# Optimization experiments

Hardware: AMD Instinct MI355X
Metric: run time of the kernel (lower is better)

The kernel has to match this reference:

```python
import jax, jax.numpy as jnp
import numpy as np

N_ATOMS = 50000
N_PAIRS = 1000000
F = 64


def setup_inputs() -> dict:
    key = jax.random.key(0)
    ks = jax.random.split(key, 9)
    return {
        "per_atom_scalar_representation": jax.random.normal(ks[0], (N_ATOMS, 1, F), dtype=jnp.float32),
        "per_atom_vector_representation": jax.random.normal(ks[1], (N_ATOMS, 3, F), dtype=jnp.float32),
        "W_ij": jax.random.normal(ks[2], (N_PAIRS, 3 * F), dtype=jnp.float32),
        "dir_ij": jax.random.normal(ks[3], (N_PAIRS, 3), dtype=jnp.float32),
        "pairlist": jax.random.randint(ks[4], (2, N_PAIRS), 0, N_ATOMS, dtype=jnp.int64),
        # interatomic_net params: Dense(F->F, silu) then Dense(F->3F)
        "W1": jax.random.normal(ks[5], (F, F), dtype=jnp.float32) / np.sqrt(F),
        "b1": jnp.zeros((F,), dtype=jnp.float32),
        "W2": jax.random.normal(ks[6], (F, 3 * F), dtype=jnp.float32) / np.sqrt(F),
        "b2": jnp.zeros((3 * F,), dtype=jnp.float32),
    }


def reference(per_atom_scalar_representation, per_atom_vector_representation,
              W_ij, dir_ij, pairlist, W1, b1, W2, b2):
    n_atoms = per_atom_scalar_representation.shape[0]
    f = W1.shape[0]
    idx_i, idx_j = pairlist[0], pairlist[1]

    # interatomic_net: Dense(F->F, silu) -> Dense(F->3F)
    h = jax.nn.silu(per_atom_scalar_representation @ W1 + b1)   # [N,1,F]
    t = h @ W2 + b2                                              # [N,1,3F]

    s_j = t[idx_j]                                               # [P,1,3F] gather
    weighted_s_j = W_ij[:, None, :] * s_j                        # [P,1,3F]
    ds1, ds2, ds3 = jnp.split(weighted_s_j, 3, axis=-1)          # each [P,1,F]

    ds_i = jax.ops.segment_sum(ds1, idx_i, num_segments=n_atoms)  # [N,1,F]
    q = per_atom_scalar_representation + ds_i

    v_j = per_atom_vector_representation[idx_j]                  # [P,3,F]
    dmu = ds2 * dir_ij[:, :, None] + ds3 * v_j                   # [P,3,F]
    dv_i = jax.ops.segment_sum(dmu, idx_i, num_segments=n_atoms)  # [N,3,F]
    mu = per_atom_vector_representation + dv_i
    return (q, mu)
```

## Files before the change

kernel.cpp:

```cpp
#include <hip/hip_runtime.h>

#define FDIM 64
#define TFDIM 192
#define MLP_A 8

static __device__ __forceinline__ float bf2f(unsigned short u) {
    union { unsigned int i; float f; } x;
    x.i = ((unsigned int)u) << 16;
    return x.f;
}
static __device__ __forceinline__ unsigned short f2bf(float f) {
    unsigned int u = __float_as_uint(f);
    unsigned int rounding = 0x7fffu + ((u >> 16) & 1u);
    return (unsigned short)((u + rounding) >> 16);
}

__global__ void zero_kernel(int* __restrict__ count, int n) {
    int i = blockIdx.x * blockDim.x + threadIdx.x;
    if (i < n) count[i] = 0;
}

__global__ void cvt_kernel(const float* __restrict__ v, unsigned short* __restrict__ v16,
                           int n_elems) {
    int g = blockIdx.x * blockDim.x + threadIdx.x;
    int n4 = n_elems >> 2;
    if (g < n4) {
        float4 x = ((const float4*)v)[g];
        ushort4 y;
        y.x = f2bf(x.x); y.y = f2bf(x.y); y.z = f2bf(x.z); y.w = f2bf(x.w);
        ((ushort4*)v16)[g] = y;
    }
}

__global__ __launch_bounds__(64) void mlp_kernel(
    const float* __restrict__ s, const float* __restrict__ W1,
    const float* __restrict__ b1, const float* __restrict__ W2,
    const float* __restrict__ b2, unsigned short* __restrict__ t16, int n_atoms) {
    __shared__ float s_lds[MLP_A][FDIM];
    __shared__ float h_lds[MLP_A][FDIM];
    const int f = threadIdx.x;
    const int atom0 = blockIdx.x * MLP_A;

#pragma unroll
    for (int a = 0; a < MLP_A; ++a) {
        int atom = atom0 + a;
        int ac = atom < n_atoms ? atom : (n_atoms - 1);
        s_lds[a][f] = s[(size_t)ac * FDIM + f];
    }
    __syncthreads();

    float acc[MLP_A];
#pragma unroll
    for (int a = 0; a < MLP_A; ++a) acc[a] = b1[f];
    for (int k = 0; k < FDIM; ++k) {
        float w = W1[k * FDIM + f];
#pragma unroll
        for (int a = 0; a < MLP_A; ++a) acc[a] = fmaf(s_lds[a][k], w, acc[a]);
    }
#pragma unroll
    for (int a = 0; a < MLP_A; ++a)
        h_lds[a][f] = acc[a] / (1.0f + __expf(-acc[a]));
    __syncthreads();

    float o0[MLP_A], o1[MLP_A], o2[MLP_A];
#pragma unroll
    for (int a = 0; a < MLP_A; ++a) {
        o0[a] = b2[f]; o1[a] = b2[FDIM + f]; o2[a] = b2[2 * FDIM + f];
    }
    for (int k = 0; k < FDIM; ++k) {
        float w0 = W2[k * TFDIM + f];
        float w1 = W2[k * TFDIM + FDIM + f];
        float w2 = W2[k * TFDIM + 2 * FDIM + f];
#pragma unroll
        for (int a = 0; a < MLP_A; ++a) {
            float h = h_lds[a][k];
            o0[a] = fmaf(h, w0, o0[a]);
            o1[a] = fmaf(h, w1, o1[a]);
            o2[a] = fmaf(h, w2, o2[a]);
        }
    }
#pragma unroll
    for (int a = 0; a < MLP_A; ++a) {
        int atom = atom0 + a;
        if (atom < n_atoms) {
            size_t base = (size_t)atom * TFDIM;
            t16[base + f] = f2bf(o0[a]);
            t16[base + FDIM + f] = f2bf(o1[a]);
            t16[base + 2 * FDIM + f] = f2bf(o2[a]);
        }
    }
}

__global__ void hist_kernel(const int* __restrict__ idx_i, int* __restrict__ count, int n_pairs) {
    int n4 = n_pairs >> 2;
    for (int g = blockIdx.x * blockDim.x + threadIdx.x; g < n4; g += gridDim.x * blockDim.x) {
        int4 ii = ((const int4*)idx_i)[g];
        atomicAdd(&count[ii.x], 1);
        atomicAdd(&count[ii.y], 1);
        atomicAdd(&count[ii.z], 1);
        atomicAdd(&count[ii.w], 1);
    }
    if (blockIdx.x == 0 && threadIdx.x == 0) {
        for (int p = n4 << 2; p < n_pairs; ++p) atomicAdd(&count[idx_i[p]], 1);
    }
}

__global__ __launch_bounds__(1024) void scan_local(const int* __restrict__ count,
                                                   int* __restrict__ offsets,
                                                   int* __restrict__ bsum, int n) {
    __shared__ int wsum[16];
    const int tid = threadIdx.x;
    const int lane = tid & 63, wid = tid >> 6;
    int i = blockIdx.x * 1024 + tid;
    int val = (i < n) ? count[i] : 0;
    int x = val;
#pragma unroll
    for (int off = 1; off < 64; off <<= 1) {
        int y = __shfl_up(x, off);
        if (lane >= off) x += y;
    }
    if (lane == 63) wsum[wid] = x;
    __syncthreads();
    if (wid == 0) {
        int w = (lane < 16) ? wsum[lane] : 0;
#pragma unroll
        for (int off = 1; off < 16; off <<= 1) {
            int y = __shfl_up(w, off);
            if (lane >= off) w += y;
        }
        if (lane < 16) wsum[lane] = w;
    }
    __syncthreads();
    int excl = x - val + (wid ? wsum[wid - 1] : 0);
    if (i < n) offsets[i] = excl;
    if (tid == 0) bsum[blockIdx.x] = wsum[15];
}

__global__ __launch_bounds__(64) void scan_tops(int* __restrict__ bsum,
                                                int* __restrict__ offsets, int nb, int n) {
    const int lane = threadIdx.x;
    int val = (lane < nb) ? bsum[lane] : 0;
    int x = val;
#pragma unroll
    for (int off = 1; off < 64; off <<= 1) {
        int y = __shfl_up(x, off);
        if (lane >= off) x += y;
    }
    if (lane < nb) bsum[lane] = x - val;
    if (lane == 63) offsets[n] = x;
}

__global__ void scan_add(int* __restrict__ offsets, const int* __restrict__ bsum, int n) {
    int i = blockIdx.x * blockDim.x + threadIdx.x;
    if (i < n) offsets[i] += bsum[i >> 10];
}

__global__ void scatter_kernel(const int* __restrict__ idx_i, const int* __restrict__ idx_j,
                               const float* __restrict__ dir, int* __restrict__ offsets,
                               int2* __restrict__ pjbuf, float4* __restrict__ dbuf,
                               int n_pairs) {
    int n4 = n_pairs >> 2;
    const float4* dir4 = (const float4*)dir;
    for (int g = blockIdx.x * blockDim.x + threadIdx.x; g < n4; g += gridDim.x * blockDim.x) {
        int4 ii = ((const int4*)idx_i)[g];
        int4 jj = ((const int4*)idx_j)[g];
        float4 da = dir4[3 * g];
        float4 db = dir4[3 * g + 1];
        float4 dc = dir4[3 * g + 2];
        int p0 = 4 * g;
        int pos;
        pos = atomicAdd(&offsets[ii.x], 1);
        pjbuf[pos] = make_int2(p0 + 0, jj.x);
        dbuf[pos] = make_float4(da.x, da.y, da.z, 0.f);
        pos = atomicAdd(&offsets[ii.y], 1);
        pjbuf[pos] = make_int2(p0 + 1, jj.y);
        dbuf[pos] = make_float4(da.w, db.x, db.y, 0.f);
        pos = atomicAdd(&offsets[ii.z], 1);
        pjbuf[pos] = make_int2(p0 + 2, jj.z);
        dbuf[pos] = make_float4(db.z, db.w, dc.x, 0.f);
        pos = atomicAdd(&offsets[ii.w], 1);
        pjbuf[pos] = make_int2(p0 + 3, jj.w);
        dbuf[pos] = make_float4(dc.y, dc.z, dc.w, 0.f);
    }
    if (blockIdx.x == 0 && threadIdx.x == 0) {
        for (int p = n4 << 2; p < n_pairs; ++p) {
            int pos = atomicAdd(&offsets[idx_i[p]], 1);
            pjbuf[pos] = make_int2(p, idx_j[p]);
            dbuf[pos] = make_float4(dir[3 * (size_t)p], dir[3 * (size_t)p + 1],
                                    dir[3 * (size_t)p + 2], 0.f);
        }
    }
}

__global__ __launch_bounds__(256) void main_kernel(
    const float* __restrict__ s, const float* __restrict__ v,
    const float* __restrict__ Wij, const unsigned short* __restrict__ v16,
    const unsigned short* __restrict__ t16, const int* __restrict__ offsets_post,
    const int* __restrict__ count, const int2* __restrict__ pjbuf,
    const float4* __restrict__ dbuf,
    float* __restrict__ q_out, float* __restrict__ mu_out, int n_atoms) {
    const int w = threadIdx.x >> 6;
    const int f = threadIdx.x & 63;
    const int i = blockIdx.x * 4 + w;
    if (i >= n_atoms) return;
    const int end = offsets_post[i];
    const int cnt = count[i];
    const int start = end - cnt;

    float accq = 0.f, acc0 = 0.f, acc1 = 0.f, acc2 = 0.f;
    for (int cbase = start; cbase < end; cbase += 64) {
        int m = end - cbase;
        if (m > 64) m = 64;
        int idx = cbase + f;
        int sidx = idx < end ? idx : start;
        int2 pj = pjbuf[sidx];
        float4 dd = dbuf[sidx];
#pragma unroll 2
        for (int k = 0; k < m; ++k) {
            int p = __builtin_amdgcn_readlane(pj.x, k);
            int j = __builtin_amdgcn_readlane(pj.y, k);
            float d0 = __uint_as_float(__builtin_amdgcn_readlane(__float_as_uint(dd.x), k));
            float d1 = __uint_as_float(__builtin_amdgcn_readlane(__float_as_uint(dd.y), k));
            float d2 = __uint_as_float(__builtin_amdgcn_readlane(__float_as_uint(dd.z), k));
            const float* wp = Wij + (size_t)p * TFDIM;
            const unsigned short* tp = t16 + (size_t)j * TFDIM;
            const unsigned short* vp = v16 + (size_t)j * TFDIM;
            float w1 = __builtin_nontemporal_load(wp + f);
            float w2 = __builtin_nontemporal_load(wp + FDIM + f);
            float w3 = __builtin_nontemporal_load(wp + 2 * FDIM + f);
            float t1 = bf2f(tp[f]);
            float t2 = bf2f(tp[FDIM + f]);
            float t3 = bf2f(tp[2 * FDIM + f]);
            float v0 = bf2f(vp[f]);
            float v1 = bf2f(vp[FDIM + f]);
            float v2 = bf2f(vp[2 * FDIM + f]);
            float ds2 = w2 * t2;
            float ds3 = w3 * t3;
            accq = fmaf(w1, t1, accq);
            acc0 = fmaf(ds2, d0, fmaf(ds3, v0, acc0));
            acc1 = fmaf(ds2, d1, fmaf(ds3, v1, acc1));
            acc2 = fmaf(ds2, d2, fmaf(ds3, v2, acc2));
        }
    }

    size_t qb = (size_t)i * FDIM;
    size_t vb = (size_t)i * TFDIM;
    __builtin_nontemporal_store(s[qb + f] + accq, &q_out[qb + f]);
    __builtin_nontemporal_store(v[vb + f] + acc0, &mu_out[vb + f]);
    __builtin_nontemporal_store(v[vb + FDIM + f] + acc1, &mu_out[vb + FDIM + f]);
    __builtin_nontemporal_store(v[vb + 2 * FDIM + f] + acc2, &mu_out[vb + 2 * FDIM + f]);
}

extern "C" void kernel_launch(void* const* d_in, const int* in_sizes, int n_in,
                              void* d_out, int out_size, void* d_ws, size_t ws_size,
                              hipStream_t stream) {
    const float* s   = (const float*)d_in[0];
    const float* v   = (const float*)d_in[1];
    const float* Wij = (const float*)d_in[2];
    const float* dir = (const float*)d_in[3];
    const int*   pl  = (const int*)d_in[4];
    const float* W1  = (const float*)d_in[5];
    const float* b1  = (const float*)d_in[6];
    const float* W2  = (const float*)d_in[7];
    const float* b2  = (const float*)d_in[8];

    const int n_atoms = in_sizes[0] / FDIM;
    const int n_pairs = in_sizes[3] / 3;
    const int* idx_i = pl;
    const int* idx_j = pl + n_pairs;

    char* ws = (char*)d_ws;
    size_t off = 0;
    auto alloc = [&](size_t bytes) {
        void* ptr = ws + off;
        off = (off + bytes + 15) & ~(size_t)15;
        return ptr;
    };
    unsigned short* t16 = (unsigned short*)alloc((size_t)n_atoms * TFDIM * 2);
    unsigned short* v16 = (unsigned short*)alloc((size_t)n_atoms * TFDIM * 2);
    int* count   = (int*)alloc((size_t)n_atoms * 4);
    int* offsets = (int*)alloc(((size_t)n_atoms + 1) * 4);
    int* bsum    = (int*)alloc(64 * 4);
    int2* pjbuf  = (int2*)alloc((size_t)n_pairs * 8);
    float4* dbuf = (float4*)alloc((size_t)n_pairs * 16);

    float* q_out  = (float*)d_out;
    float* mu_out = q_out + (size_t)n_atoms * FDIM;

    const int nb = (n_atoms + 1023) / 1024;
    const int nv = n_atoms * TFDIM;

    zero_kernel<<<(n_atoms + 255) / 256, 256, 0, stream>>>(count, n_atoms);
    cvt_kernel<<<((nv >> 2) + 255) / 256, 256, 0, stream>>>(v, v16, nv);
    mlp_kernel<<<(n_atoms + MLP_A - 1) / MLP_A, 64, 0, stream>>>(s, W1, b1, W2, b2, t16, n_atoms);
    hist_kernel<<<1024, 256, 0, stream>>>(idx_i, count, n_pairs);
    scan_local<<<nb, 1024, 0, stream>>>(count, offsets, bsum, n_atoms);
    scan_tops<<<1, 64, 0, stream>>>(bsum, offsets, nb, n_atoms);
    scan_add<<<(n_atoms + 1023) / 1024, 1024, 0, stream>>>(offsets, bsum, n_atoms);
    scatter_kernel<<<1024, 256, 0, stream>>>(idx_i, idx_j, dir, offsets, pjbuf, dbuf, n_pairs);
    main_kernel<<<(n_atoms + 3) / 4, 256, 0, stream>>>(s, v, Wij, v16, t16, offsets, count,
                                                       pjbuf, dbuf, q_out, mu_out, n_atoms);
}
```

Measured before the change: 384.3 us.

## Interleave per-atom t and v bf16 data and pack pair records into one buffer

New measurement: 432.4 us. 12.5% more time.

```diff
diff --git a/kernel.cpp b/kernel.cpp
--- a/kernel.cpp
+++ b/kernel.cpp
@@ -4,15 +4,15 @@
 #define TFDIM 192
 #define MLP_A 8
 
-static __device__ __forceinline__ float bf2f(unsigned short u) {
+static __device__ __forceinline__ float bf2f(unsigned int u16) {
     union { unsigned int i; float f; } x;
-    x.i = ((unsigned int)u) << 16;
+    x.i = u16 << 16;
     return x.f;
 }
-static __device__ __forceinline__ unsigned short f2bf(float f) {
+static __device__ __forceinline__ unsigned int f2bf(float f) {
     unsigned int u = __float_as_uint(f);
     unsigned int rounding = 0x7fffu + ((u >> 16) & 1u);
-    return (unsigned short)((u + rounding) >> 16);
+    return (u + rounding) >> 16;
 }
 
 __global__ void zero_kernel(int* __restrict__ count, int n) {
@@ -20,22 +20,11 @@
     if (i < n) count[i] = 0;
 }
 
-__global__ void cvt_kernel(const float* __restrict__ v, unsigned short* __restrict__ v16,
-                           int n_elems) {
-    int g = blockIdx.x * blockDim.x + threadIdx.x;
-    int n4 = n_elems >> 2;
-    if (g < n4) {
-        float4 x = ((const float4*)v)[g];
-        ushort4 y;
-        y.x = f2bf(x.x); y.y = f2bf(x.y); y.z = f2bf(x.z); y.w = f2bf(x.w);
-        ((ushort4*)v16)[g] = y;
-    }
-}
-
 __global__ __launch_bounds__(64) void mlp_kernel(
-    const float* __restrict__ s, const float* __restrict__ W1,
-    const float* __restrict__ b1, const float* __restrict__ W2,
-    const float* __restrict__ b2, unsigned short* __restrict__ t16, int n_atoms) {
+    const float* __restrict__ s, const float* __restrict__ v,
+    const float* __restrict__ W1, const float* __restrict__ b1,
+    const float* __restrict__ W2, const float* __restrict__ b2,
+    uint4* __restrict__ tv, int n_atoms) {
     __shared__ float s_lds[MLP_A][FDIM];
     __shared__ float h_lds[MLP_A][FDIM];
     const int f = threadIdx.x;
@@ -83,10 +72,16 @@
     for (int a = 0; a < MLP_A; ++a) {
         int atom = atom0 + a;
         if (atom < n_atoms) {
-            size_t base = (size_t)atom * TFDIM;
-            t16[base + f] = f2bf(o0[a]);
-            t16[base + FDIM + f] = f2bf(o1[a]);
-            t16[base + 2 * FDIM + f] = f2bf(o2[a]);
+            size_t vb = (size_t)atom * TFDIM;
+            float vv0 = v[vb + f];
+            float vv1 = v[vb + FDIM + f];
+            float vv2 = v[vb + 2 * FDIM + f];
+            uint4 r;
+            r.x = f2bf(o0[a]) | (f2bf(o1[a]) << 16);
+            r.y = f2bf(o2[a]) | (f2bf(vv0) << 16);
+            r.z = f2bf(vv1) | (f2bf(vv2) << 16);
+            r.w = 0u;
+            tv[(size_t)atom * FDIM + f] = r;
         }
     }
 }
@@ -157,8 +152,7 @@
 
 __global__ void scatter_kernel(const int* __restrict__ idx_i, const int* __restrict__ idx_j,
                                const float* __restrict__ dir, int* __restrict__ offsets,
-                               int2* __restrict__ pjbuf, float4* __restrict__ dbuf,
-                               int n_pairs) {
+                               int4* __restrict__ recbuf, int n_pairs) {
     int n4 = n_pairs >> 2;
     const float4* dir4 = (const float4*)dir;
     for (int g = blockIdx.x * blockDim.x + threadIdx.x; g < n4; g += gridDim.x * blockDim.x) {
@@ -170,34 +164,34 @@
         int p0 = 4 * g;
         int pos;
         pos = atomicAdd(&offsets[ii.x], 1);
-        pjbuf[pos] = make_int2(p0 + 0, jj.x);
-        dbuf[pos] = make_float4(da.x, da.y, da.z, 0.f);
+        recbuf[pos] = make_int4(p0 + 0, jj.x, (int)(f2bf(da.x) | (f2bf(da.y) << 16)),
+                                __float_as_int(da.z));
         pos = atomicAdd(&offsets[ii.y], 1);
-        pjbuf[pos] = make_int2(p0 + 1, jj.y);
-        dbuf[pos] = make_float4(da.w, db.x, db.y, 0.f);
+        recbuf[pos] = make_int4(p0 + 1, jj.y, (int)(f2bf(da.w) | (f2bf(db.x) << 16)),
+                                __float_as_int(db.y));
         pos = atomicAdd(&offsets[ii.z], 1);
-        pjbuf[pos] = make_int2(p0 + 2, jj.z);
-        dbuf[pos] = make_float4(db.z, db.w, dc.x, 0.f);
+        recbuf[pos] = make_int4(p0 + 2, jj.z, (int)(f2bf(db.z) | (f2bf(db.w) << 16)),
+                                __float_as_int(dc.x));
         pos = atomicAdd(&offsets[ii.w], 1);
-        pjbuf[pos] = make_int2(p0 + 3, jj.w);
-        dbuf[pos] = make_float4(dc.y, dc.z, dc.w, 0.f);
+        recbuf[pos] = make_int4(p0 + 3, jj.w, (int)(f2bf(dc.y) | (f2bf(dc.z) << 16)),
+                                __float_as_int(dc.w));
     }
     if (blockIdx.x == 0 && threadIdx.x == 0) {
         for (int p = n4 << 2; p < n_pairs; ++p) {
             int pos = atomicAdd(&offsets[idx_i[p]], 1);
-            pjbuf[pos] = make_int2(p, idx_j[p]);
-            dbuf[pos] = make_float4(dir[3 * (size_t)p], dir[3 * (size_t)p + 1],
-                                    dir[3 * (size_t)p + 2], 0.f);
+            recbuf[pos] = make_int4(
+                p, idx_j[p],
+                (int)(f2bf(dir[3 * (size_t)p]) | (f2bf(dir[3 * (size_t)p + 1]) << 16)),
+                __float_as_int(dir[3 * (size_t)p + 2]));
         }
     }
 }
 
 __global__ __launch_bounds__(256) void main_kernel(
     const float* __restrict__ s, const float* __restrict__ v,
-    const float* __restrict__ Wij, const unsigned short* __restrict__ v16,
-    const unsigned short* __restrict__ t16, const int* __restrict__ offsets_post,
-    const int* __restrict__ count, const int2* __restrict__ pjbuf,
-    const float4* __restrict__ dbuf,
+    const float* __restrict__ Wij, const uint4* __restrict__ tv,
+    const int* __restrict__ offsets_post, const int* __restrict__ count,
+    const int4* __restrict__ recbuf,
     float* __restrict__ q_out, float* __restrict__ mu_out, int n_atoms) {
     const int w = threadIdx.x >> 6;
     const int f = threadIdx.x & 63;
@@ -213,27 +207,26 @@
         if (m > 64) m = 64;
         int idx = cbase + f;
         int sidx = idx < end ? idx : start;
-        int2 pj = pjbuf[sidx];
-        float4 dd = dbuf[sidx];
+        int4 rec = recbuf[sidx];
 #pragma unroll 2
         for (int k = 0; k < m; ++k) {
-            int p = __builtin_amdgcn_readlane(pj.x, k);
-            int j = __builtin_amdgcn_readlane(pj.y, k);
-            float d0 = __uint_as_float(__builtin_amdgcn_readlane(__float_as_uint(dd.x), k));
-            float d1 = __uint_as_float(__builtin_amdgcn_readlane(__float_as_uint(dd.y), k));
-            float d2 = __uint_as_float(__builtin_amdgcn_readlane(__float_as_uint(dd.z), k));
+            int p = __builtin_amdgcn_readlane(rec.x, k);
+            int j = __builtin_amdgcn_readlane(rec.y, k);
+            unsigned int d01 = (unsigned int)__builtin_amdgcn_readlane(rec.z, k);
+            float d2 = __uint_as_float((unsigned int)__builtin_amdgcn_readlane(rec.w, k));
+            float d0 = bf2f(d01 & 0xffffu);
+            float d1 = bf2f(d01 >> 16);
             const float* wp = Wij + (size_t)p * TFDIM;
-            const unsigned short* tp = t16 + (size_t)j * TFDIM;
-            const unsigned short* vp = v16 + (size_t)j * TFDIM;
             float w1 = __builtin_nontemporal_load(wp + f);
             float w2 = __builtin_nontemporal_load(wp + FDIM + f);
             float w3 = __builtin_nontemporal_load(wp + 2 * FDIM + f);
-            float t1 = bf2f(tp[f]);
-            float t2 = bf2f(tp[FDIM + f]);
-            float t3 = bf2f(tp[2 * FDIM + f]);
-            float v0 = bf2f(vp[f]);
-            float v1 = bf2f(vp[FDIM + f]);
-            float v2 = bf2f(vp[2 * FDIM + f]);
+            uint4 r = tv[(size_t)j * FDIM + f];
+            float t1 = bf2f(r.x & 0xffffu);
+            float t2 = bf2f(r.x >> 16);
+            float t3 = bf2f(r.y & 0xffffu);
+            float v0 = bf2f(r.y >> 16);
+            float v1 = bf2f(r.z & 0xffffu);
+            float v2 = bf2f(r.z >> 16);
             float ds2 = w2 * t2;
             float ds3 = w3 * t3;
             accq = fmaf(w1, t1, accq);
@@ -276,28 +269,25 @@
         off = (off + bytes + 15) & ~(size_t)15;
         return ptr;
     };
-    unsigned short* t16 = (unsigned short*)alloc((size_t)n_atoms * TFDIM * 2);
-    unsigned short* v16 = (unsigned short*)alloc((size_t)n_atoms * TFDIM * 2);
+    uint4* tv    = (uint4*)alloc((size_t)n_atoms * FDIM * 16);
     int* count   = (int*)alloc((size_t)n_atoms * 4);
     int* offsets = (int*)alloc(((size_t)n_atoms + 1) * 4);
     int* bsum    = (int*)alloc(64 * 4);
-    int2* pjbuf  = (int2*)alloc((size_t)n_pairs * 8);
-    float4* dbuf = (float4*)alloc((size_t)n_pairs * 16);
+    int4* recbuf = (int4*)alloc((size_t)n_pairs * 16);
 
     float* q_out  = (float*)d_out;
     float* mu_out = q_out + (size_t)n_atoms * FDIM;
 
     const int nb = (n_atoms + 1023) / 1024;
-    const int nv = n_atoms * TFDIM;
 
     zero_kernel<<<(n_atoms + 255) / 256, 256, 0, stream>>>(count, n_atoms);
-    cvt_kernel<<<((nv >> 2) + 255) / 256, 256, 0, stream>>>(v, v16, nv);
-    mlp_kernel<<<(n_atoms + MLP_A - 1) / MLP_A, 64, 0, stream>>>(s, W1, b1, W2, b2, t16, n_atoms);
+    mlp_kernel<<<(n_atoms + MLP_A - 1) / MLP_A, 64, 0, stream>>>(s, v, W1, b1, W2, b2, tv,
+                                                                 n_atoms);
     hist_kernel<<<1024, 256, 0, stream>>>(idx_i, count, n_pairs);
     scan_local<<<nb, 1024, 0, stream>>>(count, offsets, bsum, n_atoms);
     scan_tops<<<1, 64, 0, stream>>>(bsum, offsets, nb, n_atoms);
     scan_add<<<(n_atoms + 1023) / 1024, 1024, 0, stream>>>(offsets, bsum, n_atoms);
-    scatter_kernel<<<1024, 256, 0, stream>>>(idx_i, idx_j, dir, offsets, pjbuf, dbuf, n_pairs);
-    main_kernel<<<(n_atoms + 3) / 4, 256, 0, stream>>>(s, v, Wij, v16, t16, offsets, count,
-                                                       pjbuf, dbuf, q_out, mu_out, n_atoms);
-}
+    scatter_kernel<<<1024, 256, 0, stream>>>(idx_i, idx_j, dir, offsets, recbuf, n_pairs);
+    main_kernel<<<(n_atoms + 3) / 4, 256, 0, stream>>>(s, v, Wij, tv, offsets, count, recbuf,
+                                                       q_out, mu_out, n_atoms);
+}
```
